# Kernel optimization log

Measured on AMD Instinct MI355X. Metric: run time of the kernel, lower is better.

## Reference

```python
import jax, jax.numpy as jnp
import numpy as np

HIDDEN = 1024
D_INNER = 2048      # expand * hidden
STATE = 16          # state_dim n
DT_RANK = 64        # ceil(hidden/16)
D_CONV = 4
B, S = 2, 2048
EPS = 1e-5


def setup_inputs() -> dict:
    key = jax.random.key(0)
    ks = jax.random.split(key, 10)
    sc = lambda fan_in: 1.0 / np.sqrt(fan_in)
    x = jax.random.normal(ks[0], (B, S, HIDDEN), dtype=jnp.float32)
    norm_w = jnp.ones((HIDDEN,), dtype=jnp.float32)
    in_proj_w = jax.random.uniform(ks[1], (2 * D_INNER, HIDDEN), minval=-sc(HIDDEN), maxval=sc(HIDDEN), dtype=jnp.float32)
    conv_w = jax.random.uniform(ks[2], (D_INNER, 1, D_CONV), minval=-sc(D_CONV), maxval=sc(D_CONV), dtype=jnp.float32)
    conv_b = jax.random.uniform(ks[3], (D_INNER,), minval=-sc(D_CONV), maxval=sc(D_CONV), dtype=jnp.float32)
    x_proj_w = jax.random.uniform(ks[4], (DT_RANK + 2 * STATE, D_INNER), minval=-sc(D_INNER), maxval=sc(D_INNER), dtype=jnp.float32)
    dt_proj_w = jax.random.uniform(ks[5], (D_INNER, DT_RANK), minval=-sc(DT_RANK), maxval=sc(DT_RANK), dtype=jnp.float32)
    dt_proj_b = jax.random.uniform(ks[6], (D_INNER,), minval=-sc(DT_RANK), maxval=sc(DT_RANK), dtype=jnp.float32)
    A_log = jnp.log(jnp.broadcast_to(jnp.arange(1, STATE + 1, dtype=jnp.float32), (D_INNER, STATE)))
    D = jnp.ones((D_INNER,), dtype=jnp.float32)
    out_proj_w = jax.random.uniform(ks[7], (HIDDEN, D_INNER), minval=-sc(D_INNER), maxval=sc(D_INNER), dtype=jnp.float32)
    return {"x": x, "norm_w": norm_w, "in_proj_w": in_proj_w, "conv_w": conv_w,
            "conv_b": conv_b, "x_proj_w": x_proj_w, "dt_proj_w": dt_proj_w,
            "dt_proj_b": dt_proj_b, "A_log": A_log, "D": D, "out_proj_w": out_proj_w}


def _selective_scan(u, delta, A, Bm, Cm, D):
    # u, delta: [b,s,d]; A: [d,n]; Bm, Cm: [b,s,n]; D: [d]
    deltaA = jnp.exp(jnp.einsum('bsd,dn->bsdn', delta, A))          # [b,s,d,n]
    deltaB_u = jnp.einsum('bsd,bsn,bsd->bsdn', delta, Bm, u)        # [b,s,d,n]

    def step(h, inp):
        dA_t, dBu_t, C_t = inp                                       # [b,d,n],[b,d,n],[b,n]
        h = dA_t * h + dBu_t
        y = jnp.einsum('bdn,bn->bd', h, C_t)
        return h, y

    h0 = jnp.zeros((u.shape[0], u.shape[2], A.shape[1]), dtype=u.dtype)
    _, ys = jax.lax.scan(step, h0,
                         (deltaA.transpose(1, 0, 2, 3),
                          deltaB_u.transpose(1, 0, 2, 3),
                          Cm.transpose(1, 0, 2)))
    y = ys.transpose(1, 0, 2)                                        # [b,s,d]
    return y + u * D


def reference(x, norm_w, in_proj_w, conv_w, conv_b, x_proj_w, dt_proj_w,
              dt_proj_b, A_log, D, out_proj_w):
    # RMSNorm
    xn = x * jax.lax.rsqrt(jnp.mean(x * x, axis=-1, keepdims=True) + EPS) * norm_w

    # in_proj -> split
    x_and_res = xn @ in_proj_w.T                                     # [b,s,2*d_inner]
    xi, res = jnp.split(x_and_res, 2, axis=-1)

    # causal depthwise conv1d (left-pad d_conv-1, truncate to s)
    xc = jax.lax.conv_general_dilated(
        xi.transpose(0, 2, 1), conv_w,
        window_strides=(1,), padding=[(D_CONV - 1, 0)],
        dimension_numbers=('NCH', 'OIH', 'NCH'),
        feature_group_count=D_INNER) + conv_b[None, :, None]
    xc = jax.nn.silu(xc.transpose(0, 2, 1))                          # [b,s,d_inner]

    # ssm
    A = -jnp.exp(A_log)
    x_dbl = xc @ x_proj_w.T                                          # [b,s,dt_rank+2n]
    dt, Bm, Cm = jnp.split(x_dbl, [DT_RANK, DT_RANK + STATE], axis=-1)
    delta = jax.nn.softplus(dt @ dt_proj_w.T + dt_proj_b)            # [b,s,d_inner]
    y = _selective_scan(xc, delta, A, Bm, Cm, D)

    y = y * jax.nn.silu(res)
    out = y @ out_proj_w.T
    return out + x
```

## Files before the change

### kernel.cpp

```cpp
#include <hip/hip_runtime.h>
#include <math.h>

#define HIDDEN   1024
#define D_INNER  2048
#define NSTATE   16
#define DT_RANK  64
#define BATCH    2
#define SEQ      2048
#define T_TOK    (BATCH * SEQ)
#define XDBL     (DT_RANK + 2 * NSTATE)
#define NCH      64
#define CHL      (SEQ / NCH)
#define BDN      (BATCH * D_INNER * NSTATE)

typedef float f32x4   __attribute__((ext_vector_type(4)));
typedef short bf16x8  __attribute__((ext_vector_type(8)));
typedef short short4v __attribute__((ext_vector_type(4)));

#define AS1 __attribute__((address_space(1)))
#define AS3 __attribute__((address_space(3)))
#define GLOAD(src, dst) __builtin_amdgcn_global_load_lds( \
    (const AS1 unsigned int*)(src), (AS3 unsigned int*)(dst), 16, 0, 0)

__device__ __forceinline__ float silu_f(float x) { return x / (1.0f + __expf(-x)); }
__device__ __forceinline__ float softplus_f(float x) {
    return fmaxf(x, 0.0f) + log1pf(__expf(-fabsf(x)));
}
__device__ __forceinline__ unsigned short f2bf(float x) {
    unsigned int u = __float_as_uint(x);
    u += 0x7fffu + ((u >> 16) & 1u);
    return (unsigned short)(u >> 16);
}
__device__ __forceinline__ float bf2f(unsigned short h) {
    return __uint_as_float(((unsigned int)h) << 16);
}

__device__ __forceinline__ void pack_seg(
        const float* __restrict__ w, unsigned short* __restrict__ wp,
        int K, int segs, int i) {
    int kq = K >> 2;
    int row = i / kq;
    int c = (i - row * kq) << 2;
    float4 v = *(const float4*)(w + (size_t)row * K + c);
    short4v hi, lo;
    hi.x = f2bf(v.x); hi.y = f2bf(v.y); hi.z = f2bf(v.z); hi.w = f2bf(v.w);
    lo.x = f2bf(v.x - bf2f(hi.x)); lo.y = f2bf(v.y - bf2f(hi.y));
    lo.z = f2bf(v.z - bf2f(hi.z)); lo.w = f2bf(v.w - bf2f(hi.w));
    size_t b0 = (size_t)row * (segs * K) + c;
    *(short4v*)(wp + b0) = hi;
    if (segs == 2) *(short4v*)(wp + b0 + K) = lo;
}

__global__ __launch_bounds__(256) void wpack_rms_kernel(
        const float* __restrict__ win,  unsigned short* __restrict__ pin,
        const float* __restrict__ wout, unsigned short* __restrict__ pout,
        const float* __restrict__ wx,   unsigned short* __restrict__ px,
        const float* __restrict__ wdt,  unsigned short* __restrict__ pdt,
        const float* __restrict__ x,    const float* __restrict__ nw,
        unsigned short* __restrict__ xn_p) {
    int bid = blockIdx.x;
    int t = threadIdx.x;
    if (bid < 4096) {
        pack_seg(win, pin, HIDDEN, 1, bid * 256 + t);
    } else if (bid < 6144) {
        pack_seg(wout, pout, D_INNER, 1, (bid - 4096) * 256 + t);
    } else if (bid < 6336) {
        pack_seg(wx, px, D_INNER, 2, (bid - 6144) * 256 + t);
    } else if (bid < 6464) {
        pack_seg(wdt, pdt, DT_RANK, 2, (bid - 6336) * 256 + t);
    } else {
        int row = bid - 6464;
        float4 v = ((const float4*)(x + (size_t)row * HIDDEN))[t];
        float ss = v.x*v.x + v.y*v.y + v.z*v.z + v.w*v.w;
        #pragma unroll
        for (int off = 32; off; off >>= 1) ss += __shfl_down(ss, off);
        __shared__ float wsum[4];
        if ((t & 63) == 0) wsum[t >> 6] = ss;
        __syncthreads();
        float scale = rsqrtf((wsum[0] + wsum[1] + wsum[2] + wsum[3]) / (float)HIDDEN + 1e-5f);
        float4 wv = ((const float4*)nw)[t];
        float o0 = v.x * scale * wv.x, o1 = v.y * scale * wv.y;
        float o2 = v.z * scale * wv.z, o3 = v.w * scale * wv.w;
        short4v hi, lo;
        hi.x = f2bf(o0); hi.y = f2bf(o1); hi.z = f2bf(o2); hi.w = f2bf(o3);
        lo.x = f2bf(o0 - bf2f(hi.x)); lo.y = f2bf(o1 - bf2f(hi.y));
        lo.z = f2bf(o2 - bf2f(hi.z)); lo.w = f2bf(o3 - bf2f(hi.w));
        size_t b0 = (size_t)row * (2 * HIDDEN) + t * 4;
        *(short4v*)&xn_p[b0]          = hi;
        *(short4v*)&xn_p[b0 + HIDDEN] = lo;
    }
}

template<int EPI>
__global__ __launch_bounds__(256, 2) void mgemm2_kernel(
        const unsigned short* __restrict__ Ap, int Asr, int loOff,
        const unsigned short* __restrict__ Wp, int Wsr,
        int klen, unsigned short* __restrict__ O0, unsigned short* __restrict__ O1,
        int ldout, size_t partStride) {
    __shared__ short Ah[128 * 64];
    __shared__ short Al[128 * 64];
    __shared__ short Bh[256 * 64];
    const int t = threadIdx.x;
    const int w = t >> 6, l = t & 63;
    const int m0 = blockIdx.y * 128, n0 = blockIdx.x * 256;
    const int kbeg = blockIdx.z * klen;
    const int lrow = l & 15;
    f32x4 acc[8][4];
    #pragma unroll
    for (int m = 0; m < 8; ++m)
        #pragma unroll
        for (int n = 0; n < 4; ++n) {
            acc[m][n].x = 0.f; acc[m][n].y = 0.f; acc[m][n].z = 0.f; acc[m][n].w = 0.f;
        }
    const int srow8 = l >> 3;
    const int sc8   = (l & 7) ^ srow8;
    const unsigned short* ga = Ap + (size_t)(m0 + w * 32 + srow8) * Asr + sc8 * 8;
    const unsigned short* gb = Wp + (size_t)(n0 + w * 64 + srow8) * Wsr + sc8 * 8;
    for (int k0 = kbeg; k0 < kbeg + klen; k0 += 64) {
        __syncthreads();
        #pragma unroll
        for (int q = 0; q < 4; ++q) {
            const int ar = (w * 32 + q * 8) * 128;
            GLOAD(ga + k0 + (size_t)q * 8 * Asr,         (char*)Ah + ar);
            GLOAD(ga + loOff + k0 + (size_t)q * 8 * Asr, (char*)Al + ar);
        }
        #pragma unroll
        for (int q = 0; q < 8; ++q)
            GLOAD(gb + k0 + (size_t)q * 8 * Wsr, (char*)Bh + (w * 64 + q * 8) * 128);
        __syncthreads();
        #pragma unroll
        for (int kk = 0; kk < 2; ++kk) {
            const int slot = ((kk * 4 + (l >> 4)) ^ (l & 7)) * 8;
            bf16x8 bh[4];
            #pragma unroll
            for (int n = 0; n < 4; ++n)
                bh[n] = *(const bf16x8*)&Bh[(w * 64 + n * 16 + lrow) * 64 + slot];
            #pragma unroll
            for (int m = 0; m < 8; ++m) {
                bf16x8 ah = *(const bf16x8*)&Ah[(m * 16 + lrow) * 64 + slot];
                bf16x8 al = *(const bf16x8*)&Al[(m * 16 + lrow) * 64 + slot];
                #pragma unroll
                for (int n = 0; n < 4; ++n) {
                    acc[m][n] = __builtin_amdgcn_mfma_f32_16x16x32_bf16(
                        ah, bh[n], acc[m][n], 0, 0, 0);
                    acc[m][n] = __builtin_amdgcn_mfma_f32_16x16x32_bf16(
                        al, bh[n], acc[m][n], 0, 0, 0);
                }
            }
        }
    }
    #pragma unroll
    for (int m = 0; m < 8; ++m) {
        #pragma unroll
        for (int n = 0; n < 4; ++n) {
            #pragma unroll
            for (int j = 0; j < 4; ++j) {
                int row = m0 + m * 16 + (l >> 4) * 4 + j;
                int col = n0 + w * 64 + n * 16 + (l & 15);
                float v = acc[m][n][j];
                if (EPI == 0) {
                    if (col < D_INNER) {
                        unsigned short hi = f2bf(v);
                        unsigned short lo = f2bf(v - bf2f(hi));
                        size_t o = (size_t)row * (2 * D_INNER) + col;
                        O0[o]           = hi;
                        O0[o + D_INNER] = lo;
                    } else {
                        O1[(size_t)row * D_INNER + (col - D_INNER)] = f2bf(v);
                    }
                } else {
                    O0[blockIdx.z * partStride + (size_t)row * ldout + col] = f2bf(v);
                }
            }
        }
    }
}

template<int EPI>
__global__ __launch_bounds__(256) void mgemm_kernel(
        const unsigned short* __restrict__ Ap, const unsigned short* __restrict__ Wp,
        int Klog, int klen, int brows, float* __restrict__ C0,
        int ldout, size_t partStride, const float* __restrict__ bias) {
    __shared__ short lds[4 * 128 * 64];
    short* Ah = lds;
    short* Al = lds + 128 * 64;
    short* Bh = lds + 2 * 128 * 64;
    short* Bl = lds + 3 * 128 * 64;
    const int t = threadIdx.x;
    const int w = t >> 6, l = t & 63;
    const int m0 = blockIdx.y * 128, n0 = blockIdx.x * 128;
    const int kbeg = blockIdx.z * klen;
    const int wr = (w >> 1) * 64, wc = (w & 1) * 64;
    const int lrow = l & 15;
    f32x4 acc[4][4];
    #pragma unroll
    for (int m = 0; m < 4; ++m)
        #pragma unroll
        for (int n = 0; n < 4; ++n) {
            acc[m][n].x = 0.f; acc[m][n].y = 0.f; acc[m][n].z = 0.f; acc[m][n].w = 0.f;
        }
    const int Asr = 2 * Klog;
    const int Wsr = 2 * Klog;
    const int srow = w * 32 + (l >> 3);
    const int sc8  = (l & 7) ^ ((l >> 3) & 7);
    const int brow = min(n0 + srow, brows - 1);
    const unsigned short* ga = Ap + (size_t)(m0 + srow) * Asr + sc8 * 8;
    const unsigned short* gb = Wp + (size_t)brow * Wsr + sc8 * 8;
    for (int k0 = kbeg; k0 < kbeg + klen; k0 += 64) {
        __syncthreads();
        #pragma unroll
        for (int q = 0; q < 4; ++q) {
            const int doff = (w * 32 + q * 8) * 128;
            GLOAD(ga + k0 + (size_t)q * 8 * Asr,        (char*)Ah + doff);
            GLOAD(ga + Klog + k0 + (size_t)q * 8 * Asr, (char*)Al + doff);
            GLOAD(gb + k0 + (size_t)q * 8 * Wsr,        (char*)Bh + doff);
            GLOAD(gb + Klog + k0 + (size_t)q * 8 * Wsr, (char*)Bl + doff);
        }
        __syncthreads();
        #pragma unroll
        for (int kk = 0; kk < 2; ++kk) {
            const int slot = ((kk * 4 + (l >> 4)) ^ (l & 7)) * 8;
            bf16x8 ah[4], al[4], bh[4], bl[4];
            #pragma unroll
            for (int m = 0; m < 4; ++m) {
                ah[m] = *(const bf16x8*)&Ah[(wr + m * 16 + lrow) * 64 + slot];
                al[m] = *(const bf16x8*)&Al[(wr + m * 16 + lrow) * 64 + slot];
            }
            #pragma unroll
            for (int n = 0; n < 4; ++n) {
                bh[n] = *(const bf16x8*)&Bh[(wc + n * 16 + lrow) * 64 + slot];
                bl[n] = *(const bf16x8*)&Bl[(wc + n * 16 + lrow) * 64 + slot];
            }
            #pragma unroll
            for (int m = 0; m < 4; ++m)
                #pragma unroll
                for (int n = 0; n < 4; ++n) {
                    acc[m][n] = __builtin_amdgcn_mfma_f32_16x16x32_bf16(
                        ah[m], bh[n], acc[m][n], 0, 0, 0);
                    acc[m][n] = __builtin_amdgcn_mfma_f32_16x16x32_bf16(
                        al[m], bh[n], acc[m][n], 0, 0, 0);
                    acc[m][n] = __builtin_amdgcn_mfma_f32_16x16x32_bf16(
                        ah[m], bl[n], acc[m][n], 0, 0, 0);
                }
        }
    }
    #pragma unroll
    for (int m = 0; m < 4; ++m) {
        #pragma unroll
        for (int n = 0; n < 4; ++n) {
            #pragma unroll
            for (int j = 0; j < 4; ++j) {
                int row = m0 + wr + m * 16 + (l >> 4) * 4 + j;
                int col = n0 + wc + n * 16 + (l & 15);
                float v = acc[m][n][j];
                if (EPI == 2) {
                    ((unsigned short*)C0)[blockIdx.z * partStride
                        + (size_t)row * ldout + col] = f2bf(v);
                } else {
                    C0[(size_t)row * ldout + col] = softplus_f(v + bias[col]);
                }
            }
        }
    }
}

__global__ __launch_bounds__(256) void reduce4_kernel(
        const unsigned short* __restrict__ parts, size_t partStride,
        const float* __restrict__ x, float* __restrict__ out) {
    size_t i = (size_t)blockIdx.x * 256 + threadIdx.x;
    short4v a = *(const short4v*)(parts + i * 4);
    short4v b = *(const short4v*)(parts + partStride + i * 4);
    short4v c = *(const short4v*)(parts + 2 * partStride + i * 4);
    short4v d = *(const short4v*)(parts + 3 * partStride + i * 4);
    float4 xv = ((const float4*)x)[i];
    float4 o;
    o.x = bf2f(a.x) + bf2f(b.x) + bf2f(c.x) + bf2f(d.x) + xv.x;
    o.y = bf2f(a.y) + bf2f(b.y) + bf2f(c.y) + bf2f(d.y) + xv.y;
    o.z = bf2f(a.z) + bf2f(b.z) + bf2f(c.z) + bf2f(d.z) + xv.z;
    o.w = bf2f(a.w) + bf2f(b.w) + bf2f(c.w) + bf2f(d.w) + xv.w;
    ((float4*)out)[i] = o;
}

__global__ __launch_bounds__(256) void reduceX_kernel(
        const unsigned short* __restrict__ parts, float* __restrict__ xdbl,
        unsigned short* __restrict__ dtp) {
    int i = blockIdx.x * 256 + threadIdx.x;
    int row = i / 24;
    int c = (i - row * 24) * 4;
    float s0 = 0.f, s1 = 0.f, s2 = 0.f, s3 = 0.f;
    #pragma unroll
    for (int z = 0; z < 8; ++z) {
        short4v a = *(const short4v*)(parts + (size_t)z * 524288 + (size_t)row * 128 + c);
        s0 += bf2f(a.x); s1 += bf2f(a.y); s2 += bf2f(a.z); s3 += bf2f(a.w);
    }
    *(float4*)(xdbl + (size_t)row * XDBL + c) = make_float4(s0, s1, s2, s3);
    if (c < DT_RANK) {
        short4v hi, lo;
        hi.x = f2bf(s0); hi.y = f2bf(s1); hi.z = f2bf(s2); hi.w = f2bf(s3);
        lo.x = f2bf(s0 - bf2f(hi.x)); lo.y = f2bf(s1 - bf2f(hi.y));
        lo.z = f2bf(s2 - bf2f(hi.z)); lo.w = f2bf(s3 - bf2f(hi.w));
        size_t b0 = (size_t)row * 128 + c;
        *(short4v*)(dtp + b0)      = hi;
        *(short4v*)(dtp + b0 + 64) = lo;
    }
}

__global__ __launch_bounds__(256) void conv_silu_kernel(
        const unsigned short* __restrict__ xi_p, const float* __restrict__ w,
        const float* __restrict__ b, unsigned short* __restrict__ xc_p) {
    size_t i = (size_t)blockIdx.x * 256 + threadIdx.x;
    int d = (int)(i & (D_INNER - 1));
    int tt = (int)(i >> 11);
    int s = tt & (SEQ - 1);
    float4 wv = ((const float4*)w)[d];
    float acc = b[d];
    #pragma unroll
    for (int k = 3; k >= 1; --k) {
        if (s >= k) {
            size_t o = (size_t)(tt - k) * (2 * D_INNER) + d;
            float u = bf2f(xi_p[o]) + bf2f(xi_p[o + D_INNER]);
            acc += ((const float*)&wv)[3 - k] * u;
        }
    }
    {
        size_t o = (size_t)tt * (2 * D_INNER) + d;
        float u = bf2f(xi_p[o]) + bf2f(xi_p[o + D_INNER]);
        acc += wv.w * u;
    }
    float o = silu_f(acc);
    unsigned short hi = f2bf(o);
    unsigned short lo = f2bf(o - bf2f(hi));
    size_t o2 = (size_t)tt * (2 * D_INNER) + d;
    xc_p[o2]           = hi;
    xc_p[o2 + D_INNER] = lo;
}


__global__ __launch_bounds__(256) void scanA_kernel(
        const unsigned short* __restrict__ xcp, const float* __restrict__ delta,
        const float* __restrict__ xdbl, const float* __restrict__ A_log,
        float* __restrict__ hpart, float* __restrict__ Pp) {
    __shared__ float sB[CHL * NSTATE];
    const int bid = blockIdx.x;
    const int b    = bid >> 9;
    const int c    = (bid >> 3) & 63;
    const int dblk = bid & 7;
    const int d    = (dblk << 8) + threadIdx.x;
    const int rowbase = b * SEQ + c * CHL;
    #pragma unroll
    for (int q = 0; q < 2; ++q) {
        int e = threadIdx.x + q * 256;
        int r = e >> 4, n = e & 15;
        sB[e] = xdbl[(size_t)(rowbase + r) * XDBL + DT_RANK + n];
    }
    float adn[NSTATE];
    #pragma unroll
    for (int k = 0; k < 4; ++k) {
        float4 a = *(const float4*)(A_log + d * NSTATE + k * 4);
        adn[k*4+0] = -__expf(a.x); adn[k*4+1] = -__expf(a.y);
        adn[k*4+2] = -__expf(a.z); adn[k*4+3] = -__expf(a.w);
    }
    float h[NSTATE], P[NSTATE];
    #pragma unroll
    for (int n = 0; n < NSTATE; ++n) { h[n] = 0.f; P[n] = 1.f; }
    __syncthreads();
    #pragma unroll 4
    for (int r = 0; r < CHL; ++r) {
        const int row = rowbase + r;
        const float* brow = &sB[r * NSTATE];
        size_t o2 = (size_t)row * (2 * D_INNER) + d;
        float dl = delta[(size_t)row * D_INNER + d];
        float u  = bf2f(xcp[o2]) + bf2f(xcp[o2 + D_INNER]);
        float du = dl * u;
        #pragma unroll
        for (int n = 0; n < NSTATE; ++n) {
            float dA = __expf(dl * adn[n]);
            h[n] = fmaf(dA, h[n], du * brow[n]);
            P[n] *= dA;
        }
    }
    size_t base = (size_t)c * BDN + (size_t)(b * D_INNER + d) * NSTATE;
    #pragma unroll
    for (int k = 0; k < 4; ++k) {
        *(float4*)(hpart + base + k * 4) = make_float4(h[k*4], h[k*4+1], h[k*4+2], h[k*4+3]);
        *(float4*)(Pp    + base + k * 4) = make_float4(P[k*4], P[k*4+1], P[k*4+2], P[k*4+3]);
    }
}

__global__ __launch_bounds__(256) void scanB_kernel(
        float* __restrict__ hpart, const float* __restrict__ Pp) {
    int idx = blockIdx.x * 256 + threadIdx.x;
    float h = 0.f;
    for (int c = 0; c < NCH; ++c) {
        size_t o = (size_t)c * BDN + idx;
        float hp = hpart[o];
        float p  = Pp[o];
        hpart[o] = h;
        h = fmaf(p, h, hp);
    }
}

__global__ __launch_bounds__(256) void scanC_kernel(
        const unsigned short* xcp, const float* __restrict__ delta,
        const float* __restrict__ xdbl, const float* __restrict__ A_log,
        const float* __restrict__ Dp, const float* __restrict__ hstart,
        const unsigned short* __restrict__ res_b, unsigned short* y_p) {
    __shared__ float sB[CHL * NSTATE];
    __shared__ float sC[CHL * NSTATE];
    const int bid = blockIdx.x;
    const int b    = bid >> 9;
    const int c    = (bid >> 3) & 63;
    const int dblk = bid & 7;
    const int d    = (dblk << 8) + threadIdx.x;
    const int rowbase = b * SEQ + c * CHL;
    #pragma unroll
    for (int q = 0; q < 2; ++q) {
        int e = threadIdx.x + q * 256;
        int r = e >> 4, n = e & 15;
        sB[e] = xdbl[(size_t)(rowbase + r) * XDBL + DT_RANK + n];
        sC[e] = xdbl[(size_t)(rowbase + r) * XDBL + DT_RANK + NSTATE + n];
    }
    float adn[NSTATE];
    #pragma unroll
    for (int k = 0; k < 4; ++k) {
        float4 a = *(const float4*)(A_log + d * NSTATE + k * 4);
        adn[k*4+0] = -__expf(a.x); adn[k*4+1] = -__expf(a.y);
        adn[k*4+2] = -__expf(a.z); adn[k*4+3] = -__expf(a.w);
    }
    const float Dd = Dp[d];
    float h[NSTATE];
    size_t base = (size_t)c * BDN + (size_t)(b * D_INNER + d) * NSTATE;
    #pragma unroll
    for (int k = 0; k < 4; ++k) {
        float4 hv = *(const float4*)(hstart + base + k * 4);
        h[k*4] = hv.x; h[k*4+1] = hv.y; h[k*4+2] = hv.z; h[k*4+3] = hv.w;
    }
    __syncthreads();
    #pragma unroll 4
    for (int r = 0; r < CHL; ++r) {
        const int row = rowbase + r;
        const float* brow = &sB[r * NSTATE];
        const float* crow = &sC[r * NSTATE];
        size_t o2 = (size_t)row * (2 * D_INNER) + d;
        float dl = delta[(size_t)row * D_INNER + d];
        float u  = bf2f(xcp[o2]) + bf2f(xcp[o2 + D_INNER]);
        float du = dl * u;
        float ys[4];
        ys[0] = u * Dd; ys[1] = 0.f; ys[2] = 0.f; ys[3] = 0.f;
        #pragma unroll
        for (int n = 0; n < NSTATE; ++n) {
            float dA = __expf(dl * adn[n]);
            h[n] = fmaf(dA, h[n], du * brow[n]);
            ys[n & 3] = fmaf(h[n], crow[n], ys[n & 3]);
        }
        float ysum = (ys[0] + ys[1]) + (ys[2] + ys[3]);
        float rv = bf2f(res_b[(size_t)row * D_INNER + d]);
        float gv = ysum * silu_f(rv);
        unsigned short hi = f2bf(gv);
        unsigned short lo = f2bf(gv - bf2f(hi));
        y_p[o2]           = hi;
        y_p[o2 + D_INNER] = lo;
    }
}

extern "C" void kernel_launch(void* const* d_in, const int* in_sizes, int n_in,
                              void* d_out, int out_size, void* d_ws, size_t ws_size,
                              hipStream_t stream) {
    const float* x         = (const float*)d_in[0];
    const float* norm_w    = (const float*)d_in[1];
    const float* in_proj_w = (const float*)d_in[2];
    const float* conv_w    = (const float*)d_in[3];
    const float* conv_b    = (const float*)d_in[4];
    const float* x_proj_w  = (const float*)d_in[5];
    const float* dt_proj_w = (const float*)d_in[6];
    const float* dt_proj_b = (const float*)d_in[7];
    const float* A_log     = (const float*)d_in[8];
    const float* Dp        = (const float*)d_in[9];
    const float* out_proj_w= (const float*)d_in[10];
    float* out = (float*)d_out;
    float* ws  = (float*)d_ws;

    const size_t M8 = (size_t)T_TOK * D_INNER;
    unsigned short* res_b  = (unsigned short*)ws;
    unsigned short* parts_b= (unsigned short*)ws;
    float* delta = ws + M8;
    float* xdbl  = delta + M8;
    unsigned short* xn_p   = (unsigned short*)(xdbl + (size_t)T_TOK * XDBL);
    unsigned short* w_in_p = xn_p   + (size_t)4096 * 2048;
    unsigned short* w_out_p= w_in_p + (size_t)4096 * 1024;
    unsigned short* w_xp_p = w_out_p+ (size_t)1024 * 2048;
    unsigned short* w_dt_p = w_xp_p + (size_t)96 * 4096;
    unsigned short* xc_p   = w_dt_p + (size_t)2048 * 128;
    unsigned short* dtp_p  = xc_p   + (size_t)4096 * 4096;
    unsigned short* xi_p   = dtp_p + (size_t)4096 * 128;
    float* hpart = (float*)xi_p;
    float* Pp    = hpart + (size_t)BDN * NCH;
    unsigned short* parts_x = (unsigned short*)delta;
    unsigned short* y_p = xc_p;
    const size_t partStride = (size_t)T_TOK * HIDDEN;

    wpack_rms_kernel<<<6464 + T_TOK, 256, 0, stream>>>(
        in_proj_w, w_in_p, out_proj_w, w_out_p, x_proj_w, w_xp_p,
        dt_proj_w, w_dt_p, x, norm_w, xn_p);

    {
        dim3 g(4096 / 256, T_TOK / 128, 1);
        mgemm2_kernel<0><<<g, 256, 0, stream>>>(xn_p, 2 * HIDDEN, HIDDEN,
                                                w_in_p, HIDDEN, HIDDEN,
                                                xi_p, res_b, 0, 0);
    }

    conv_silu_kernel<<<(int)(M8 / 256), 256, 0, stream>>>(xi_p, conv_w, conv_b, xc_p);

    {
        dim3 g(1, T_TOK / 128, 8);
        mgemm_kernel<2><<<g, 256, 0, stream>>>(xc_p, w_xp_p, D_INNER, D_INNER / 8,
                                               96, (float*)parts_x, 128, 524288, nullptr);
    }
    reduceX_kernel<<<T_TOK * 24 / 256, 256, 0, stream>>>(parts_x, xdbl, dtp_p);

    {
        dim3 g(D_INNER / 128, T_TOK / 128, 1);
        mgemm_kernel<3><<<g, 256, 0, stream>>>(dtp_p, w_dt_p, DT_RANK, DT_RANK,
                                               D_INNER, delta, D_INNER, 0, dt_proj_b);
    }

    scanA_kernel<<<BATCH * NCH * 8, 256, 0, stream>>>(xc_p, delta, xdbl, A_log, hpart, Pp);
    scanB_kernel<<<BDN / 256, 256, 0, stream>>>(hpart, Pp);
    scanC_kernel<<<BATCH * NCH * 8, 256, 0, stream>>>(xc_p, delta, xdbl, A_log, Dp,
                                                      hpart, res_b, y_p);

    {
        dim3 g(HIDDEN / 256, T_TOK / 128, 4);
        mgemm2_kernel<2><<<g, 256, 0, stream>>>(y_p, 2 * D_INNER, D_INNER,
                                                w_out_p, D_INNER, D_INNER / 4,
                                                parts_b, nullptr, HIDDEN, partStride);
    }
    reduce4_kernel<<<(int)(partStride / 4 / 256), 256, 0, stream>>>(parts_b, partStride, x, out);
}
```

Measured before the change: 288.2 us.

## Double-buffer split-bf16 GEMMs with 256x256 tiles and concatenated K packing

```diff
diff --git a/kernel.cpp b/kernel.cpp
--- a/kernel.cpp
+++ b/kernel.cpp
@@ -35,20 +35,25 @@
     return __uint_as_float(((unsigned int)h) << 16);
 }
 
+template<int MODE>
 __device__ __forceinline__ void pack_seg(
         const float* __restrict__ w, unsigned short* __restrict__ wp,
-        int K, int segs, int i) {
+        int K, int i) {
     int kq = K >> 2;
     int row = i / kq;
     int c = (i - row * kq) << 2;
     float4 v = *(const float4*)(w + (size_t)row * K + c);
     short4v hi, lo;
     hi.x = f2bf(v.x); hi.y = f2bf(v.y); hi.z = f2bf(v.z); hi.w = f2bf(v.w);
-    lo.x = f2bf(v.x - bf2f(hi.x)); lo.y = f2bf(v.y - bf2f(hi.y));
-    lo.z = f2bf(v.z - bf2f(hi.z)); lo.w = f2bf(v.w - bf2f(hi.w));
-    size_t b0 = (size_t)row * (segs * K) + c;
+    size_t b0 = (size_t)row * (2 * K) + c;
     *(short4v*)(wp + b0) = hi;
-    if (segs == 2) *(short4v*)(wp + b0 + K) = lo;
+    if (MODE == 1) {
+        *(short4v*)(wp + b0 + K) = hi;
+    } else {
+        lo.x = f2bf(v.x - bf2f(hi.x)); lo.y = f2bf(v.y - bf2f(hi.y));
+        lo.z = f2bf(v.z - bf2f(hi.z)); lo.w = f2bf(v.w - bf2f(hi.w));
+        *(short4v*)(wp + b0 + K) = lo;
+    }
 }
 
 __global__ __launch_bounds__(256) void wpack_rms_kernel(
@@ -61,13 +66,13 @@
     int bid = blockIdx.x;
     int t = threadIdx.x;
     if (bid < 4096) {
-        pack_seg(win, pin, HIDDEN, 1, bid * 256 + t);
+        pack_seg<1>(win, pin, HIDDEN, bid * 256 + t);
     } else if (bid < 6144) {
-        pack_seg(wout, pout, D_INNER, 1, (bid - 4096) * 256 + t);
+        pack_seg<1>(wout, pout, D_INNER, (bid - 4096) * 256 + t);
     } else if (bid < 6336) {
-        pack_seg(wx, px, D_INNER, 2, (bid - 6144) * 256 + t);
+        pack_seg<0>(wx, px, D_INNER, (bid - 6144) * 256 + t);
     } else if (bid < 6464) {
-        pack_seg(wdt, pdt, DT_RANK, 2, (bid - 6336) * 256 + t);
+        pack_seg<0>(wdt, pdt, DT_RANK, (bid - 6336) * 256 + t);
     } else {
         int row = bid - 6464;
         float4 v = ((const float4*)(x + (size_t)row * HIDDEN))[t];
@@ -92,18 +97,17 @@
 }
 
 template<int EPI>
-__global__ __launch_bounds__(256, 2) void mgemm2_kernel(
-        const unsigned short* __restrict__ Ap, int Asr, int loOff,
-        const unsigned short* __restrict__ Wp, int Wsr,
-        int klen, unsigned short* __restrict__ O0, unsigned short* __restrict__ O1,
+__global__ __launch_bounds__(512, 2) void mgemmP_kernel(
+        const unsigned short* __restrict__ Ap, const unsigned short* __restrict__ Wp,
+        int Kp, int klen, unsigned short* __restrict__ O0, unsigned short* __restrict__ O1,
         int ldout, size_t partStride) {
-    __shared__ short Ah[128 * 64];
-    __shared__ short Al[128 * 64];
-    __shared__ short Bh[256 * 64];
+    __shared__ char lds8[131072];
     const int t = threadIdx.x;
     const int w = t >> 6, l = t & 63;
-    const int m0 = blockIdx.y * 128, n0 = blockIdx.x * 256;
+    const int wm = w >> 2, wn = w & 3;
+    const int m0 = blockIdx.y * 256, n0 = blockIdx.x * 256;
     const int kbeg = blockIdx.z * klen;
+    const int NT = klen >> 6;
     const int lrow = l & 15;
     f32x4 acc[8][4];
     #pragma unroll
@@ -112,41 +116,68 @@
         for (int n = 0; n < 4; ++n) {
             acc[m][n].x = 0.f; acc[m][n].y = 0.f; acc[m][n].z = 0.f; acc[m][n].w = 0.f;
         }
-    const int srow8 = l >> 3;
-    const int sc8   = (l & 7) ^ srow8;
-    const unsigned short* ga = Ap + (size_t)(m0 + w * 32 + srow8) * Asr + sc8 * 8;
-    const unsigned short* gb = Wp + (size_t)(n0 + w * 64 + srow8) * Wsr + sc8 * 8;
-    for (int k0 = kbeg; k0 < kbeg + klen; k0 += 64) {
-        __syncthreads();
+    const int sc8 = (l & 7) ^ ((l >> 3) & 7);
+    const unsigned short* gA = Ap + (size_t)(m0 + w * 8 + (l >> 3)) * Kp + kbeg + sc8 * 8;
+    const unsigned short* gB = Wp + (size_t)(n0 + w * 8 + (l >> 3)) * Kp + kbeg + sc8 * 8;
+    auto stage = [&](int buf, int tile) {
+        const int koff = tile * 64;
         #pragma unroll
         for (int q = 0; q < 4; ++q) {
-            const int ar = (w * 32 + q * 8) * 128;
-            GLOAD(ga + k0 + (size_t)q * 8 * Asr,         (char*)Ah + ar);
-            GLOAD(ga + loOff + k0 + (size_t)q * 8 * Asr, (char*)Al + ar);
-        }
-        #pragma unroll
-        for (int q = 0; q < 8; ++q)
-            GLOAD(gb + k0 + (size_t)q * 8 * Wsr, (char*)Bh + (w * 64 + q * 8) * 128);
-        __syncthreads();
-        #pragma unroll
-        for (int kk = 0; kk < 2; ++kk) {
-            const int slot = ((kk * 4 + (l >> 4)) ^ (l & 7)) * 8;
-            bf16x8 bh[4];
+            GLOAD(gA + koff + (size_t)(q * 64) * Kp,
+                  lds8 + buf * 32768 + q * 8192 + w * 1024);
+            GLOAD(gB + koff + (size_t)(q * 64) * Kp,
+                  lds8 + 65536 + buf * 32768 + q * 8192 + w * 1024);
+        }
+    };
+    stage(0, 0);
+    stage(1, 1);
+    asm volatile("s_waitcnt vmcnt(8)" ::: "memory");
+    __builtin_amdgcn_s_barrier();
+    for (int tt = 0; tt < NT; ++tt) {
+        const int cur = tt & 1;
+        const char* Ab = lds8 + cur * 32768;
+        const char* Bb = lds8 + 65536 + cur * 32768;
+        const int sl0 = (((l >> 4)    ) ^ (l & 7)) * 16;
+        const int sl1 = (((l >> 4) + 4) ^ (l & 7)) * 16;
+        {
+            bf16x8 bh[4], af[8];
             #pragma unroll
             for (int n = 0; n < 4; ++n)
-                bh[n] = *(const bf16x8*)&Bh[(w * 64 + n * 16 + lrow) * 64 + slot];
-            #pragma unroll
-            for (int m = 0; m < 8; ++m) {
-                bf16x8 ah = *(const bf16x8*)&Ah[(m * 16 + lrow) * 64 + slot];
-                bf16x8 al = *(const bf16x8*)&Al[(m * 16 + lrow) * 64 + slot];
+                bh[n] = *(const bf16x8*)(Bb + (wn * 64 + n * 16 + lrow) * 128 + sl0);
+            #pragma unroll
+            for (int m = 0; m < 8; ++m)
+                af[m] = *(const bf16x8*)(Ab + (wm * 128 + m * 16 + lrow) * 128 + sl0);
+            #pragma unroll
+            for (int m = 0; m < 8; ++m)
                 #pragma unroll
-                for (int n = 0; n < 4; ++n) {
+                for (int n = 0; n < 4; ++n)
                     acc[m][n] = __builtin_amdgcn_mfma_f32_16x16x32_bf16(
-                        ah, bh[n], acc[m][n], 0, 0, 0);
-                    acc[m][n] = __builtin_amdgcn_mfma_f32_16x16x32_bf16(
-                        al, bh[n], acc[m][n], 0, 0, 0);
-                }
-            }
+                        af[m], bh[n], acc[m][n], 0, 0, 0);
+        }
+        bf16x8 bh1[4], af1[8];
+        #pragma unroll
+        for (int n = 0; n < 4; ++n)
+            bh1[n] = *(const bf16x8*)(Bb + (wn * 64 + n * 16 + lrow) * 128 + sl1);
+        #pragma unroll
+        for (int m = 0; m < 8; ++m)
+            af1[m] = *(const bf16x8*)(Ab + (wm * 128 + m * 16 + lrow) * 128 + sl1);
+        if (tt < NT - 1) {
+            asm volatile("s_waitcnt lgkmcnt(0)" ::: "memory");
+            __builtin_amdgcn_s_barrier();
+            if (tt + 2 < NT) stage(cur, tt + 2);
+        }
+        #pragma unroll
+        for (int m = 0; m < 8; ++m)
+            #pragma unroll
+            for (int n = 0; n < 4; ++n)
+                acc[m][n] = __builtin_amdgcn_mfma_f32_16x16x32_bf16(
+                    af1[m], bh1[n], acc[m][n], 0, 0, 0);
+        if (tt < NT - 1) {
+            if (tt + 2 < NT)
+                asm volatile("s_waitcnt vmcnt(8)" ::: "memory");
+            else
+                asm volatile("s_waitcnt vmcnt(0)" ::: "memory");
+            __builtin_amdgcn_s_barrier();
         }
     }
     #pragma unroll
@@ -155,8 +186,8 @@
         for (int n = 0; n < 4; ++n) {
             #pragma unroll
             for (int j = 0; j < 4; ++j) {
-                int row = m0 + m * 16 + (l >> 4) * 4 + j;
-                int col = n0 + w * 64 + n * 16 + (l & 15);
+                int row = m0 + wm * 128 + m * 16 + (l >> 4) * 4 + j;
+                int col = n0 + wn * 64 + n * 16 + (l & 15);
                 float v = acc[m][n][j];
                 if (EPI == 0) {
                     if (col < D_INNER) {
@@ -487,8 +518,8 @@
     float* xdbl  = delta + M8;
     unsigned short* xn_p   = (unsigned short*)(xdbl + (size_t)T_TOK * XDBL);
     unsigned short* w_in_p = xn_p   + (size_t)4096 * 2048;
-    unsigned short* w_out_p= w_in_p + (size_t)4096 * 1024;
-    unsigned short* w_xp_p = w_out_p+ (size_t)1024 * 2048;
+    unsigned short* w_out_p= w_in_p + (size_t)4096 * 2048;
+    unsigned short* w_xp_p = w_out_p+ (size_t)1024 * 4096;
     unsigned short* w_dt_p = w_xp_p + (size_t)96 * 4096;
     unsigned short* xc_p   = w_dt_p + (size_t)2048 * 128;
     unsigned short* dtp_p  = xc_p   + (size_t)4096 * 4096;
@@ -504,9 +535,8 @@
         dt_proj_w, w_dt_p, x, norm_w, xn_p);
 
     {
-        dim3 g(4096 / 256, T_TOK / 128, 1);
-        mgemm2_kernel<0><<<g, 256, 0, stream>>>(xn_p, 2 * HIDDEN, HIDDEN,
-                                                w_in_p, HIDDEN, HIDDEN,
+        dim3 g(4096 / 256, T_TOK / 256, 1);
+        mgemmP_kernel<0><<<g, 512, 0, stream>>>(xn_p, w_in_p, 2048, 2048,
                                                 xi_p, res_b, 0, 0);
     }
 
@@ -531,9 +561,8 @@
                                                       hpart, res_b, y_p);
 
     {
-        dim3 g(HIDDEN / 256, T_TOK / 128, 4);
-        mgemm2_kernel<2><<<g, 256, 0, stream>>>(y_p, 2 * D_INNER, D_INNER,
-                                                w_out_p, D_INNER, D_INNER / 4,
+        dim3 g(HIDDEN / 256, T_TOK / 256, 4);
+        mgemmP_kernel<2><<<g, 512, 0, stream>>>(y_p, w_out_p, 4096, 1024,
                                                 parts_b, nullptr, HIDDEN, partStride);
     }
     reduce4_kernel<<<(int)(partStride / 4 / 256), 256, 0, stream>>>(parts_b, partStride, x, out);
```

Measured after the change: 291.4 us. About the same (+1.1%).
